# Performance work log

Hardware: AMD Instinct MI355X
Metric: run time of the kernel (lower is better)

## Reference

```python
import jax, jax.numpy as jnp
import numpy as np

N, E = 100000, 800000
D_IN, D_H, D_EMB = 64, 64, 64
L, S = 2, 4
NOISE_SCALE, MIN_U = 0.1, 1e-6


def _xavier(k, shape):
    lim = float(np.sqrt(6.0 / (shape[0] + shape[1])))
    return jax.random.uniform(k, shape, jnp.float32, -lim, lim)


def setup_inputs():
    key = jax.random.key(0)
    ks = jax.random.split(key, 7)
    x = jax.random.normal(ks[0], (N, D_IN), jnp.float32)
    edge_index = jax.random.randint(ks[1], (2, E), 0, N)
    parent_mask = jax.random.bernoulli(ks[2], 0.7, (E,))
    Wi = _xavier(ks[3], (D_IN, D_H))
    bi = jnp.zeros((D_H,), jnp.float32)
    msg_W = jnp.stack([_xavier(jax.random.fold_in(ks[4], l), (2 * D_H, D_H)) for l in range(L)])
    msg_b = jnp.zeros((L, D_H), jnp.float32)
    upd_W = jnp.stack([_xavier(jax.random.fold_in(ks[5], l), (2 * D_H, D_H)) for l in range(L)])
    upd_b = jnp.zeros((L, D_H), jnp.float32)
    Wf = _xavier(ks[6], (D_H, D_EMB))
    bf = jnp.zeros((D_EMB,), jnp.float32)
    return dict(x=x, edge_index=edge_index, parent_mask=parent_mask, Wi=Wi, bi=bi,
                msg_W=msg_W, msg_b=msg_b, upd_W=upd_W, upd_b=upd_b, Wf=Wf, bf=bf)


def _gnn(x, src, dst, mask_f, cnt_inv, Wi, bi, msg_W, msg_b, upd_W, upd_b, Wf, bf):
    # input_proj -> relu, then L rounds of (gather -> message linear -> masked
    # scatter-mean -> update linear -> relu), then final_proj.
    h = jax.nn.relu(x @ Wi + bi)
    for l in range(L):
        Wm, Wu = msg_W[l], upd_W[l]
        # message = Linear(concat(x_i, x_j)); x_i = h[dst] (target), x_j = h[src] (source)
        msg = h[dst] @ Wm[:D_H] + h[src] @ Wm[D_H:] + msg_b[l]  # [E, D_H]
        agg = jax.ops.segment_sum(msg * mask_f[:, None], dst, num_segments=N) * cnt_inv[:, None]
        # update = Linear(concat(x, aggr_out))
        h = jax.nn.relu(h @ Wu[:D_H] + agg @ Wu[D_H:] + upd_b[l])
    return h @ Wf + bf  # [N, D_EMB]


def reference(x, edge_index, parent_mask, Wi, bi, msg_W, msg_b, upd_W, upd_b, Wf, bf):
    src, dst = edge_index[0], edge_index[1]
    mask_f = parent_mask.astype(x.dtype)
    # scatter-mean over causal-parent edges only (0 for nodes without parents, as in PyG)
    cnt = jax.ops.segment_sum(mask_f, dst, num_segments=N)
    cnt_inv = 1.0 / jnp.maximum(cnt, 1.0)
    params = (Wi, bi, msg_W, msg_b, upd_W, upd_b, Wf, bf)
    causal_z = _gnn(x, src, dst, mask_f, cnt_inv, *params)
    # Monte Carlo uncertainty: S perturbed causal embeddings, trace of sample covariance
    noise = jax.random.normal(jax.random.key(42), (S, N, D_IN), x.dtype) * NOISE_SCALE
    zs = jax.lax.map(lambda n: _gnn(x + n, src, dst, mask_f, cnt_inv, *params), noise)  # [S, N, D_EMB]
    mean = zs.mean(axis=0)
    u = jnp.sum((zs - mean[None]) ** 2, axis=(0, 2)) / (S - 1)
    u = jnp.maximum(u, MIN_U)
    return causal_z, u
```

## Files before the change

kernel.cpp:

```cpp
#include <hip/hip_runtime.h>
#include <stdint.h>

#define NN 100000
#define EE 800000
#define GEMM_BX 1563
#define WSTR 72
#define SLAB ((size_t)NN * 64)
#define EDGE_CAP 2304

typedef unsigned short u16;
typedef __attribute__((ext_vector_type(8))) short bf16x8;
typedef __attribute__((ext_vector_type(4))) float f32x4;

__device__ __forceinline__ uint32_t f2bf(float f) {
  uint32_t u = __float_as_uint(f);
  return (u + 0x7fffu + ((u >> 16) & 1u)) >> 16;
}

__device__ __forceinline__ void tf_round(uint32_t& x0, uint32_t& x1, int r) {
  x0 += x1;
  x1 = (x1 << r) | (x1 >> (32 - r));
  x1 ^= x0;
}

__device__ __forceinline__ void threefry_0_42(uint32_t c0, uint32_t c1,
                                              uint32_t& o0, uint32_t& o1) {
  const uint32_t ks0 = 0u, ks1 = 42u, ks2 = 0x1BD11BDAu ^ 42u;
  uint32_t x0 = c0 + ks0, x1 = c1 + ks1;
  tf_round(x0, x1, 13); tf_round(x0, x1, 15); tf_round(x0, x1, 26); tf_round(x0, x1, 6);
  x0 += ks1; x1 += ks2 + 1u;
  tf_round(x0, x1, 17); tf_round(x0, x1, 29); tf_round(x0, x1, 16); tf_round(x0, x1, 24);
  x0 += ks2; x1 += ks0 + 2u;
  tf_round(x0, x1, 13); tf_round(x0, x1, 15); tf_round(x0, x1, 26); tf_round(x0, x1, 6);
  x0 += ks0; x1 += ks1 + 3u;
  tf_round(x0, x1, 17); tf_round(x0, x1, 29); tf_round(x0, x1, 16); tf_round(x0, x1, 24);
  x0 += ks1; x1 += ks2 + 4u;
  tf_round(x0, x1, 13); tf_round(x0, x1, 15); tf_round(x0, x1, 26); tf_round(x0, x1, 6);
  x0 += ks2; x1 += ks0 + 5u;
  o0 = x0; o1 = x1;
}

__device__ __forceinline__ float noise_val(int s, int n, int d) {
  uint32_t f = (uint32_t)s * 6400000u + (uint32_t)n * 64u + (uint32_t)d;
  uint32_t o0, o1;
  threefry_0_42(0u, f, o0, o1);
  uint32_t bits = o0 ^ o1;
  float v = __uint_as_float((bits >> 9) | 0x3f800000u) - 1.0f;
  const float LO = -0.99999994f;
  float u = v * 2.0f + LO;
  u = fmaxf(u, LO);
  float w = -__logf(fmaf(-u, u, 1.0f));
  float ww = w - 2.5f;
  float p = 2.81022636e-08f;
  p = fmaf(p, ww, 3.43273939e-07f);
  p = fmaf(p, ww, -3.5233877e-06f);
  p = fmaf(p, ww, -4.39150654e-06f);
  p = fmaf(p, ww, 0.00021858087f);
  p = fmaf(p, ww, -0.00125372503f);
  p = fmaf(p, ww, -0.00417768164f);
  p = fmaf(p, ww, 0.246640727f);
  p = fmaf(p, ww, 1.50140941f);
  if (__any(w >= 5.0f)) {
    float ws = sqrtf(w) - 3.0f;
    float p2 = -0.000200214257f;
    p2 = fmaf(p2, ws, 0.000100950558f);
    p2 = fmaf(p2, ws, 0.00134934322f);
    p2 = fmaf(p2, ws, -0.00367342844f);
    p2 = fmaf(p2, ws, 0.00573950773f);
    p2 = fmaf(p2, ws, -0.0076224613f);
    p2 = fmaf(p2, ws, 0.00943887047f);
    p2 = fmaf(p2, ws, 1.00167406f);
    p2 = fmaf(p2, ws, 2.83297682f);
    p = (w < 5.0f) ? p : p2;
  }
  return 0.141421356f * (p * u);
}

__device__ __forceinline__ int mask_at(const void* m, int e, int mode) {
  if (mode == 0) return ((const int*)m)[e] != 0;
  if (mode == 1) return ((const unsigned char*)m)[e] != 0;
  return ((const float*)m)[e] != 0.0f;
}

__global__ void k_detect(const unsigned* mw, int* mode_out) {
  __shared__ int nonbin, nonfloat;
  if (threadIdx.x == 0) { nonbin = 0; nonfloat = 0; }
  __syncthreads();
  int lb = 0, lf = 0;
  for (int i = threadIdx.x; i < 4096; i += 256) {
    unsigned v = mw[i];
    if (v > 1u) lb = 1;
    if (v != 0u && v != 0x3F800000u) lf = 1;
  }
  if (lb) atomicOr(&nonbin, 1);
  if (lf) atomicOr(&nonfloat, 1);
  __syncthreads();
  if (threadIdx.x == 0)
    mode_out[0] = (nonbin == 0) ? 0 : ((nonfloat == 0) ? 2 : 1);
}

__global__ void k_count(const void* mask, const int* dst, int* cnt, const int* mode_p) {
  int e = blockIdx.x * 256 + threadIdx.x;
  if (e >= EE) return;
  if (mask_at(mask, e, *mode_p)) atomicAdd(&cnt[dst[e]], 1);
}

__global__ void k_scan_a(const int* cnt, int* blockSums) {
  __shared__ int sd[256];
  int t = threadIdx.x;
  int base = blockIdx.x * 1024 + t * 4;
  int s = 0;
  #pragma unroll
  for (int j = 0; j < 4; ++j) {
    int i = base + j;
    if (i < NN) s += cnt[i];
  }
  sd[t] = s;
  __syncthreads();
  for (int off = 128; off > 0; off >>= 1) {
    if (t < off) sd[t] += sd[t + off];
    __syncthreads();
  }
  if (t == 0) blockSums[blockIdx.x] = sd[0];
}

__global__ void k_scan_b(int* blockSums, int nb, int* total_out) {
  __shared__ int sd[128];
  int t = threadIdx.x;
  int v = (t < nb) ? blockSums[t] : 0;
  sd[t] = v;
  __syncthreads();
  for (int off = 1; off < 128; off <<= 1) {
    int x = (t >= off) ? sd[t - off] : 0;
    __syncthreads();
    sd[t] += x;
    __syncthreads();
  }
  if (t < nb) blockSums[t] = sd[t] - v;
  if (t == 0) total_out[0] = sd[127];
}

__global__ void k_scan_c(const int* cnt, const int* blockOffs, int* row_ptr,
                         int* cursor, float* cinv) {
  __shared__ int sd[256];
  int t = threadIdx.x;
  int base = blockIdx.x * 1024 + t * 4;
  int v[4], s = 0;
  #pragma unroll
  for (int j = 0; j < 4; ++j) {
    int i = base + j;
    v[j] = (i < NN) ? cnt[i] : 0;
    s += v[j];
  }
  sd[t] = s;
  __syncthreads();
  for (int off = 1; off < 256; off <<= 1) {
    int x = (t >= off) ? sd[t - off] : 0;
    __syncthreads();
    sd[t] += x;
    __syncthreads();
  }
  int excl = sd[t] - s + blockOffs[blockIdx.x];
  #pragma unroll
  for (int j = 0; j < 4; ++j) {
    int i = base + j;
    if (i < NN) {
      row_ptr[i] = excl;
      cursor[i] = excl;
      cinv[i] = 1.0f / fmaxf((float)v[j], 1.0f);
    }
    excl += v[j];
  }
}

__global__ void k_fill(const void* mask, const int* src, const int* dst,
                       int* cursor, int* col, const int* mode_p) {
  int e = blockIdx.x * 256 + threadIdx.x;
  if (e >= EE) return;
  if (mask_at(mask, e, *mode_p)) {
    int p = atomicAdd(&cursor[dst[e]], 1);
    col[p] = src[e];
  }
}

__global__ void k_prep(const float* msg_W, const float* msg_b, const float* upd_W,
                       const float* Wi, const float* Wf,
                       u16* Wu1T, u16* A1T, u16* A2T, float* C1,
                       u16* WiT, u16* WfT) {
  int t = threadIdx.x;
  int blk = blockIdx.x;
  if (blk >= 128) {
    const float* W = (blk == 128) ? Wi : Wf;
    u16* WT = (blk == 128) ? WiT : WfT;
    for (int o = t; o < 4096; o += 256) {
      int k = o >> 6, n = o & 63;
      WT[n * 64 + k] = (u16)f2bf(W[k * 64 + n]);
    }
    int l = blk - 128;
    const float* Wu2 = upd_W + l * 8192 + 4096;
    if (t < 64) {
      float acc = 0.f;
      for (int j = 0; j < 64; ++j) acc = fmaf(msg_b[l * 64 + j], Wu2[j * 64 + t], acc);
      C1[l * 64 + t] = acc;
    }
    return;
  }
  int l = blk >> 6, b = blk & 63;
  const float* WmT = msg_W + l * 8192;
  const float* WmB = WmT + 4096;
  const float* Wu1 = upd_W + l * 8192;
  const float* Wu2 = Wu1 + 4096;
  __shared__ float sd1[256], sd2[256];
  int a = t & 63, part = t >> 6;
  float a1 = 0.f, a2 = 0.f;
  #pragma unroll
  for (int jj = 0; jj < 16; ++jj) {
    int j = part * 16 + jj;
    float w2 = Wu2[j * 64 + b];
    a1 = fmaf(WmT[a * 64 + j], w2, a1);
    a2 = fmaf(WmB[a * 64 + j], w2, a2);
  }
  sd1[part * 64 + a] = a1;
  sd2[part * 64 + a] = a2;
  __syncthreads();
  if (t < 64) {
    float s1 = sd1[t] + sd1[64 + t] + sd1[128 + t] + sd1[192 + t];
    float s2 = sd2[t] + sd2[64 + t] + sd2[128 + t] + sd2[192 + t];
    int o = l * 4096 + b * 64 + t;
    A1T[o] = (u16)f2bf(s1);
    A2T[o] = (u16)f2bf(s2);
    Wu1T[o] = (u16)f2bf(Wu1[t * 64 + b]);
  }
}

__device__ __forceinline__ void mm4(const u16* lW, int m16, int q,
                                    bf16x8 a0, bf16x8 a1, f32x4 (&acc)[4]) {
  #pragma unroll
  for (int nt = 0; nt < 4; ++nt) {
    const u16* wp = lW + (nt * 16 + m16) * WSTR + q * 8;
    bf16x8 b0 = *(const bf16x8*)(wp);
    bf16x8 b1 = *(const bf16x8*)(wp + 32);
    acc[nt] = __builtin_amdgcn_mfma_f32_16x16x32_bf16(a0, b0, acc[nt], 0, 0, 0);
    acc[nt] = __builtin_amdgcn_mfma_f32_16x16x32_bf16(a1, b1, acc[nt], 0, 0, 0);
  }
}

__device__ __forceinline__ void stage_W(const u16* __restrict__ WT, u16* lW) {
  int t = threadIdx.x;
  int r = t >> 2, seg = (t & 3) * 16;
  const uint4* p = (const uint4*)(WT + r * 64 + seg);
  uint4 a = p[0], b = p[1];
  *(uint4*)(lW + r * WSTR + seg) = a;
  *(uint4*)(lW + r * WSTR + seg + 8) = b;
}

__device__ __forceinline__ void stage_H(const u16* __restrict__ Hin, int R0, u16* lT) {
  int t = threadIdx.x;
  int r = t >> 2, seg = (t & 3) * 16;
  int gr = R0 + r;
  uint4 a = {0, 0, 0, 0}, b = {0, 0, 0, 0};
  if (gr < NN) {
    const uint4* p = (const uint4*)(Hin + (size_t)gr * 64 + seg);
    a = p[0]; b = p[1];
  }
  *(uint4*)(lT + r * WSTR + seg) = a;
  *(uint4*)(lT + r * WSTR + seg + 8) = b;
}

__global__ __launch_bounds__(256) void k_input(const float* __restrict__ x,
                                               const u16* __restrict__ WiT,
                                               const float* __restrict__ bi,
                                               u16* __restrict__ HoutB) {
  __shared__ __align__(16) u16 lT[64 * WSTR];
  __shared__ __align__(16) u16 lW[64 * WSTR];
  __shared__ float lB[64];
  int t = threadIdx.x;
  int R0 = blockIdx.x * 64;
  int inst = blockIdx.y;
  u16* Hout = HoutB + (size_t)inst * SLAB;
  {
    int r = t >> 2, seg = (t & 3) * 16;
    int gr = R0 + r;
    float v[16];
    if (gr < NN) {
      const float4* xp = (const float4*)(x + (size_t)gr * 64 + seg);
      #pragma unroll
      for (int qq = 0; qq < 4; ++qq) {
        float4 f = xp[qq];
        v[qq * 4 + 0] = f.x; v[qq * 4 + 1] = f.y;
        v[qq * 4 + 2] = f.z; v[qq * 4 + 3] = f.w;
      }
      if (inst > 0) {
        int s = inst - 1;
        #pragma unroll
        for (int j = 0; j < 16; ++j) v[j] += noise_val(s, gr, seg + j);
      }
    } else {
      #pragma unroll
      for (int j = 0; j < 16; ++j) v[j] = 0.f;
    }
    uint32_t pk[8];
    #pragma unroll
    for (int j = 0; j < 8; ++j)
      pk[j] = f2bf(v[2 * j]) | (f2bf(v[2 * j + 1]) << 16);
    uint4 A = {pk[0], pk[1], pk[2], pk[3]};
    uint4 B = {pk[4], pk[5], pk[6], pk[7]};
    *(uint4*)(lT + r * WSTR + seg) = A;
    *(uint4*)(lT + r * WSTR + seg + 8) = B;
  }
  stage_W(WiT, lW);
  if (t < 64) lB[t] = bi[t];
  __syncthreads();
  int l = t & 63, w = t >> 6;
  int m16 = l & 15, q = l >> 4;
  const u16* aRow = lT + (w * 16 + m16) * WSTR + q * 8;
  bf16x8 fa0 = *(const bf16x8*)(aRow);
  bf16x8 fa1 = *(const bf16x8*)(aRow + 32);
  f32x4 acc[4] = {{0.f, 0.f, 0.f, 0.f}, {0.f, 0.f, 0.f, 0.f},
                  {0.f, 0.f, 0.f, 0.f}, {0.f, 0.f, 0.f, 0.f}};
  mm4(lW, m16, q, fa0, fa1, acc);
  #pragma unroll
  for (int nt = 0; nt < 4; ++nt) {
    int c = nt * 16 + m16;
    #pragma unroll
    for (int r_ = 0; r_ < 4; ++r_) {
      int row = w * 16 + q * 4 + r_;
      int gr = R0 + row;
      if (gr < NN) {
        float vv = fmaxf(acc[nt][r_] + lB[c], 0.f);
        Hout[(size_t)gr * 64 + c] = (u16)f2bf(vv);
      }
    }
  }
}

__global__ __launch_bounds__(256) void k_layer(const u16* __restrict__ HinB,
                                               u16* __restrict__ HoutB,
                                               const int* __restrict__ row_ptr,
                                               const int* __restrict__ col,
                                               const float* __restrict__ cinv,
                                               const u16* __restrict__ Wu1T,
                                               const u16* __restrict__ A1T,
                                               const u16* __restrict__ A2T,
                                               const float* __restrict__ b0,
                                               const float* __restrict__ c1) {
  __shared__ __align__(16) u16 lS0[64 * WSTR];
  __shared__ __align__(16) u16 lS1[64 * WSTR];
  __shared__ __align__(16) u16 lW[64 * WSTR];
  __shared__ float lB[128];
  __shared__ float lG[64];
  __shared__ int   lRP[65];
  int* lEdge = (int*)lW;

  int t = threadIdx.x;
  int R0 = blockIdx.x * 64;
  int instBase = blockIdx.y * 2;
  bool two = (instBase + 1) < 5;
  const u16* Hin0 = HinB + (size_t)instBase * SLAB;
  const u16* Hin1 = Hin0 + (two ? SLAB : 0);
  u16* Hout0 = HoutB + (size_t)instBase * SLAB;
  u16* Hout1 = Hout0 + SLAB;

  if (t < 65) {
    int idx = R0 + t;
    if (idx > NN) idx = NN;
    lRP[t] = row_ptr[idx];
  }
  if (t < 64) {
    lB[t] = b0[t];
    lB[64 + t] = c1[t];
  }
  __syncthreads();

  int e0 = lRP[0];
  int nE = lRP[64] - e0;
  bool inLds = (nE <= EDGE_CAP);
  if (inLds) {
    for (int i = t; i < nE; i += 256) lEdge[i] = col[e0 + i];
  }
  if (t < 64) lG[t] = (lRP[t + 1] > lRP[t]) ? 1.f : 0.f;
  __syncthreads();

  {
    int sub = t >> 3, lane8 = t & 7;
    int f0 = lane8 * 8;
    const u16* hb0 = Hin0 + f0;
    const u16* hb1 = Hin1 + f0;
    #pragma unroll
    for (int bb = 0; bb < 2; ++bb) {
      int r = bb * 32 + sub;
      int n = R0 + r;
      float g[8], h[8];
      #pragma unroll
      for (int j = 0; j < 8; ++j) { g[j] = 0.f; h[j] = 0.f; }
      if (n < NN) {
        int e = lRP[r], end = lRP[r + 1];
        int last = end - 1;
        for (; e < end; e += 4) {
          int idx4[4];
          #pragma unroll
          for (int j = 0; j < 4; ++j) {
            int ee = e + j;
            ee = (ee < last) ? ee : last;
            idx4[j] = inLds ? lEdge[ee - e0] : col[ee];
          }
          uint4 P[4];
          #pragma unroll
          for (int j = 0; j < 4; ++j)
            P[j] = *(const uint4*)(hb0 + ((unsigned)idx4[j] << 6));
          uint4 Q[4];
          if (two) {
            #pragma unroll
            for (int j = 0; j < 4; ++j)
              Q[j] = *(const uint4*)(hb1 + ((unsigned)idx4[j] << 6));
          }
          #pragma unroll
          for (int j = 1; j < 4; ++j) {
            bool ok = (e + j) < end;
            P[j].x = ok ? P[j].x : 0u;
            P[j].y = ok ? P[j].y : 0u;
            P[j].z = ok ? P[j].z : 0u;
            P[j].w = ok ? P[j].w : 0u;
            if (two) {
              Q[j].x = ok ? Q[j].x : 0u;
              Q[j].y = ok ? Q[j].y : 0u;
              Q[j].z = ok ? Q[j].z : 0u;
              Q[j].w = ok ? Q[j].w : 0u;
            }
          }
          #pragma unroll
          for (int j = 0; j < 4; ++j) {
            uint4 v = P[j];
            g[0] += __uint_as_float(v.x << 16);
            g[1] += __uint_as_float(v.x & 0xffff0000u);
            g[2] += __uint_as_float(v.y << 16);
            g[3] += __uint_as_float(v.y & 0xffff0000u);
            g[4] += __uint_as_float(v.z << 16);
            g[5] += __uint_as_float(v.z & 0xffff0000u);
            g[6] += __uint_as_float(v.w << 16);
            g[7] += __uint_as_float(v.w & 0xffff0000u);
          }
          if (two) {
            #pragma unroll
            for (int j = 0; j < 4; ++j) {
              uint4 v = Q[j];
              h[0] += __uint_as_float(v.x << 16);
              h[1] += __uint_as_float(v.x & 0xffff0000u);
              h[2] += __uint_as_float(v.y << 16);
              h[3] += __uint_as_float(v.y & 0xffff0000u);
              h[4] += __uint_as_float(v.z << 16);
              h[5] += __uint_as_float(v.z & 0xffff0000u);
              h[6] += __uint_as_float(v.w << 16);
              h[7] += __uint_as_float(v.w & 0xffff0000u);
            }
          }
        }
        float ci = cinv[n];
        #pragma unroll
        for (int j = 0; j < 8; ++j) { g[j] *= ci; h[j] *= ci; }
      }
      uint4 pk;
      pk.x = f2bf(g[0]) | (f2bf(g[1]) << 16);
      pk.y = f2bf(g[2]) | (f2bf(g[3]) << 16);
      pk.z = f2bf(g[4]) | (f2bf(g[5]) << 16);
      pk.w = f2bf(g[6]) | (f2bf(g[7]) << 16);
      *(uint4*)(lS0 + r * WSTR + f0) = pk;
      if (two) {
        uint4 pk2;
        pk2.x = f2bf(h[0]) | (f2bf(h[1]) << 16);
        pk2.y = f2bf(h[2]) | (f2bf(h[3]) << 16);
        pk2.z = f2bf(h[4]) | (f2bf(h[5]) << 16);
        pk2.w = f2bf(h[6]) | (f2bf(h[7]) << 16);
        *(uint4*)(lS1 + r * WSTR + f0) = pk2;
      }
    }
  }
  __syncthreads();

  int l = t & 63, w = t >> 6;
  int m16 = l & 15, q = l >> 4;
  int arow = w * 16 + m16;
  int gra = R0 + arow;
  bf16x8 zz = {0, 0, 0, 0, 0, 0, 0, 0};
  bf16x8 fa0_0 = zz, fa1_0 = zz, fa0_1 = zz, fa1_1 = zz;
  if (gra < NN) {
    const u16* ap = Hin0 + (size_t)gra * 64 + q * 8;
    fa0_0 = *(const bf16x8*)(ap);
    fa1_0 = *(const bf16x8*)(ap + 32);
    if (two) {
      const u16* ap1 = Hin1 + (size_t)gra * 64 + q * 8;
      fa0_1 = *(const bf16x8*)(ap1);
      fa1_1 = *(const bf16x8*)(ap1 + 32);
    }
  }

  stage_W(Wu1T, lW);
  __syncthreads();

  float gA = lG[arow];
  f32x4 acc0[4] = {{0.f, 0.f, 0.f, 0.f}, {0.f, 0.f, 0.f, 0.f},
                   {0.f, 0.f, 0.f, 0.f}, {0.f, 0.f, 0.f, 0.f}};
  f32x4 acc1[4] = {{0.f, 0.f, 0.f, 0.f}, {0.f, 0.f, 0.f, 0.f},
                   {0.f, 0.f, 0.f, 0.f}, {0.f, 0.f, 0.f, 0.f}};
  mm4(lW, m16, q, fa0_0, fa1_0, acc0);
  if (two) mm4(lW, m16, q, fa0_1, fa1_1, acc1);
  __syncthreads();
  stage_W(A1T, lW);
  __syncthreads();
  {
    bf16x8 ga0 = (gA != 0.f) ? fa0_0 : zz;
    bf16x8 ga1 = (gA != 0.f) ? fa1_0 : zz;
    mm4(lW, m16, q, ga0, ga1, acc0);
    if (two) {
      bf16x8 gb0 = (gA != 0.f) ? fa0_1 : zz;
      bf16x8 gb1 = (gA != 0.f) ? fa1_1 : zz;
      mm4(lW, m16, q, gb0, gb1, acc1);
    }
  }
  __syncthreads();
  stage_W(A2T, lW);
  __syncthreads();
  {
    const u16* sRow = lS0 + arow * WSTR + q * 8;
    bf16x8 fs0 = *(const bf16x8*)(sRow);
    bf16x8 fs1 = *(const bf16x8*)(sRow + 32);
    mm4(lW, m16, q, fs0, fs1, acc0);
    if (two) {
      const u16* sRow1 = lS1 + arow * WSTR + q * 8;
      bf16x8 ft0 = *(const bf16x8*)(sRow1);
      bf16x8 ft1 = *(const bf16x8*)(sRow1 + 32);
      mm4(lW, m16, q, ft0, ft1, acc1);
    }
  }
  #pragma unroll
  for (int nt = 0; nt < 4; ++nt) {
    int c = nt * 16 + m16;
    #pragma unroll
    for (int r_ = 0; r_ < 4; ++r_) {
      int row = w * 16 + q * 4 + r_;
      int gr = R0 + row;
      if (gr < NN) {
        float bias = lB[c] + lG[row] * lB[64 + c];
        float v0 = fmaxf(acc0[nt][r_] + bias, 0.f);
        Hout0[(size_t)gr * 64 + c] = (u16)f2bf(v0);
        if (two) {
          float v1 = fmaxf(acc1[nt][r_] + bias, 0.f);
          Hout1[(size_t)gr * 64 + c] = (u16)f2bf(v1);
        }
      }
    }
  }
}

__global__ __launch_bounds__(256) void k_final(const u16* __restrict__ HinB,
                                               const u16* __restrict__ WfT,
                                               const float* __restrict__ bfv,
                                               float* __restrict__ outCausal,
                                               float* __restrict__ out_u) {
  __shared__ __align__(16) u16 lT[64 * WSTR];
  __shared__ __align__(16) u16 lW[64 * WSTR];
  __shared__ float lB[64];
  int t = threadIdx.x;
  int R0 = blockIdx.x * 64;
  stage_W(WfT, lW);
  if (t < 64) lB[t] = bfv[t];
  int l = t & 63, w = t >> 6;
  int m16 = l & 15, q = l >> 4;
  float s1[16], s2[16];
  #pragma unroll
  for (int j = 0; j < 16; ++j) { s1[j] = 0.f; s2[j] = 0.f; }

  for (int inst = 0; inst < 5; ++inst) {
    __syncthreads();
    stage_H(HinB + (size_t)inst * SLAB, R0, lT);
    __syncthreads();
    const u16* aRow = lT + (w * 16 + m16) * WSTR + q * 8;
    bf16x8 fa0 = *(const bf16x8*)(aRow);
    bf16x8 fa1 = *(const bf16x8*)(aRow + 32);
    f32x4 acc[4] = {{0.f, 0.f, 0.f, 0.f}, {0.f, 0.f, 0.f, 0.f},
                    {0.f, 0.f, 0.f, 0.f}, {0.f, 0.f, 0.f, 0.f}};
    mm4(lW, m16, q, fa0, fa1, acc);
    #pragma unroll
    for (int nt = 0; nt < 4; ++nt) {
      int c = nt * 16 + m16;
      #pragma unroll
      for (int r_ = 0; r_ < 4; ++r_) {
        float z = acc[nt][r_] + lB[c];
        if (inst == 0) {
          int gr = R0 + w * 16 + q * 4 + r_;
          if (gr < NN) outCausal[(size_t)gr * 64 + c] = z;
        } else {
          s1[nt * 4 + r_] += z;
          s2[nt * 4 + r_] = fmaf(z, z, s2[nt * 4 + r_]);
        }
      }
    }
  }
  #pragma unroll
  for (int r_ = 0; r_ < 4; ++r_) {
    float pr = 0.f;
    #pragma unroll
    for (int nt = 0; nt < 4; ++nt) {
      float a = s1[nt * 4 + r_];
      pr += s2[nt * 4 + r_] - 0.25f * a * a;
    }
    #pragma unroll
    for (int msk = 1; msk < 16; msk <<= 1)
      pr += __shfl_xor(pr, msk, 64);
    if (m16 == 0) {
      int gr = R0 + w * 16 + q * 4 + r_;
      if (gr < NN) out_u[gr] = fmaxf(pr * (1.0f / 3.0f), 1e-6f);
    }
  }
}

extern "C" void kernel_launch(void* const* d_in, const int* in_sizes, int n_in,
                              void* d_out, int out_size, void* d_ws, size_t ws_size,
                              hipStream_t stream) {
  const float* x      = (const float*)d_in[0];
  const int*   eidx   = (const int*)d_in[1];
  const void*  mask   = d_in[2];
  const float* Wi     = (const float*)d_in[3];
  const float* bi     = (const float*)d_in[4];
  const float* msg_W  = (const float*)d_in[5];
  const float* msg_b  = (const float*)d_in[6];
  const float* upd_W  = (const float*)d_in[7];
  const float* upd_b  = (const float*)d_in[8];
  const float* Wf     = (const float*)d_in[9];
  const float* bfv    = (const float*)d_in[10];

  const int* src = eidx;
  const int* dst = eidx + EE;

  char* ws = (char*)d_ws;
  size_t off = 0;
  auto alloc = [&](size_t bytes) -> void* {
    void* p = ws + off;
    off += (bytes + 255) & ~(size_t)255;
    return p;
  };

  int*   cnt     = (int*)alloc(NN * sizeof(int));
  float* cinv    = (float*)alloc(NN * sizeof(float));
  int*   row_ptr = (int*)alloc((NN + 1) * sizeof(int));
  int*   cursor  = (int*)alloc(NN * sizeof(int));
  int*   col     = (int*)alloc(EE * sizeof(int));
  int*   bsums   = (int*)alloc(128 * sizeof(int));
  int*   mode_p  = (int*)alloc(sizeof(int));
  u16*   Wu1T    = (u16*)alloc(2 * 4096 * sizeof(u16));
  u16*   A1T     = (u16*)alloc(2 * 4096 * sizeof(u16));
  u16*   A2T     = (u16*)alloc(2 * 4096 * sizeof(u16));
  u16*   WiT     = (u16*)alloc(4096 * sizeof(u16));
  u16*   WfT     = (u16*)alloc(4096 * sizeof(u16));
  float* C1      = (float*)alloc(2 * 64 * sizeof(float));
  u16*   HA      = (u16*)alloc(5 * SLAB * sizeof(u16));
  u16*   HB      = (u16*)alloc(5 * SLAB * sizeof(u16));

  float* out_causal = (float*)d_out;
  float* out_u      = (float*)d_out + SLAB;

  k_detect<<<1, 256, 0, stream>>>((const unsigned*)mask, mode_p);
  hipMemsetAsync(cnt, 0, NN * sizeof(int), stream);
  k_count<<<EE / 256, 256, 0, stream>>>(mask, dst, cnt, mode_p);
  const int SCAN_BLKS = (NN + 1023) / 1024;
  k_scan_a<<<SCAN_BLKS, 256, 0, stream>>>(cnt, bsums);
  k_scan_b<<<1, 128, 0, stream>>>(bsums, SCAN_BLKS, row_ptr + NN);
  k_scan_c<<<SCAN_BLKS, 256, 0, stream>>>(cnt, bsums, row_ptr, cursor, cinv);
  k_fill<<<EE / 256, 256, 0, stream>>>(mask, src, dst, cursor, col, mode_p);

  k_prep<<<130, 256, 0, stream>>>(msg_W, msg_b, upd_W, Wi, Wf,
                                  Wu1T, A1T, A2T, C1, WiT, WfT);

  dim3 g5(GEMM_BX, 5);
  dim3 gl(GEMM_BX, 3);
  k_input<<<g5, 256, 0, stream>>>(x, WiT, bi, HA);
  k_layer<<<gl, 256, 0, stream>>>(HA, HB, row_ptr, col, cinv,
                                  Wu1T, A1T, A2T, upd_b, C1);
  k_layer<<<gl, 256, 0, stream>>>(HB, HA, row_ptr, col, cinv,
                                  Wu1T + 4096, A1T + 4096, A2T + 4096,
                                  upd_b + 64, C1 + 64);
  k_final<<<GEMM_BX, 256, 0, stream>>>(HA, WfT, bfv, out_causal, out_u);

  (void)in_sizes; (void)n_in; (void)out_size; (void)ws_size;
}
```

Baseline: 434.4 us.

## Fuse CSR build passes with input projection into interleaved mega-kernels

Merges the edge-count atomics with the first input-projection tiles and the weight-prep work into one launch, and the CSR fill atomics with the remaining input-projection tiles into a second launch. Even and odd blocks are interleaved so memory-bound atomic work and MFMA-based projection tiles can run on the GPU at the same time. Small prep work (mode detect, Wi/Wf transpose, C1) moves into a tiny pre-kernel. The input-projection loading is also rewritten to read x straight into MFMA fragment registers instead of staging through LDS. This cuts launch count and idle tails but adds divergent block roles and more complex index mapping.

```diff
diff --git a/kernel.cpp b/kernel.cpp
--- a/kernel.cpp
+++ b/kernel.cpp
@@ -7,6 +7,9 @@
 #define WSTR 72
 #define SLAB ((size_t)NN * 64)
 #define EDGE_CAP 2304
+
+#define MA_TOTAL 6379
+#define MB_TOTAL 7814
 
 typedef unsigned short u16;
 typedef __attribute__((ext_vector_type(8))) short bf16x8;
@@ -82,27 +85,44 @@
   return ((const float*)m)[e] != 0.0f;
 }
 
-__global__ void k_detect(const unsigned* mw, int* mode_out) {
-  __shared__ int nonbin, nonfloat;
-  if (threadIdx.x == 0) { nonbin = 0; nonfloat = 0; }
-  __syncthreads();
-  int lb = 0, lf = 0;
-  for (int i = threadIdx.x; i < 4096; i += 256) {
-    unsigned v = mw[i];
-    if (v > 1u) lb = 1;
-    if (v != 0u && v != 0x3F800000u) lf = 1;
-  }
-  if (lb) atomicOr(&nonbin, 1);
-  if (lf) atomicOr(&nonfloat, 1);
-  __syncthreads();
-  if (threadIdx.x == 0)
-    mode_out[0] = (nonbin == 0) ? 0 : ((nonfloat == 0) ? 2 : 1);
-}
-
-__global__ void k_count(const void* mask, const int* dst, int* cnt, const int* mode_p) {
-  int e = blockIdx.x * 256 + threadIdx.x;
-  if (e >= EE) return;
-  if (mask_at(mask, e, *mode_p)) atomicAdd(&cnt[dst[e]], 1);
+__global__ void k_pre(const unsigned* mw, int* mode_out,
+                      const float* Wi, const float* Wf,
+                      const float* msg_b, const float* upd_W,
+                      u16* WiT, u16* WfT, float* C1) {
+  int b = blockIdx.x, t = threadIdx.x;
+  if (b == 0) {
+    __shared__ int nonbin, nonfloat;
+    if (t == 0) { nonbin = 0; nonfloat = 0; }
+    __syncthreads();
+    int lb = 0, lf = 0;
+    for (int i = t; i < 4096; i += 256) {
+      unsigned v = mw[i];
+      if (v > 1u) lb = 1;
+      if (v != 0u && v != 0x3F800000u) lf = 1;
+    }
+    if (lb) atomicOr(&nonbin, 1);
+    if (lf) atomicOr(&nonfloat, 1);
+    __syncthreads();
+    if (t == 0)
+      mode_out[0] = (nonbin == 0) ? 0 : ((nonfloat == 0) ? 2 : 1);
+    return;
+  }
+  if (b <= 2) {
+    const float* W = (b == 1) ? Wi : Wf;
+    u16* WT = (b == 1) ? WiT : WfT;
+    for (int o = t; o < 4096; o += 256) {
+      int k = o >> 6, n = o & 63;
+      WT[n * 64 + k] = (u16)f2bf(W[k * 64 + n]);
+    }
+    return;
+  }
+  int l = b - 3;
+  const float* Wu2 = upd_W + l * 8192 + 4096;
+  if (t < 64) {
+    float acc = 0.f;
+    for (int j = 0; j < 64; ++j) acc = fmaf(msg_b[l * 64 + j], Wu2[j * 64 + t], acc);
+    C1[l * 64 + t] = acc;
+  }
 }
 
 __global__ void k_scan_a(const int* cnt, int* blockSums) {
@@ -173,44 +193,135 @@
   }
 }
 
-__global__ void k_fill(const void* mask, const int* src, const int* dst,
-                       int* cursor, int* col, const int* mode_p) {
-  int e = blockIdx.x * 256 + threadIdx.x;
-  if (e >= EE) return;
-  if (mask_at(mask, e, *mode_p)) {
-    int p = atomicAdd(&cursor[dst[e]], 1);
-    col[p] = src[e];
-  }
-}
-
-__global__ void k_prep(const float* msg_W, const float* msg_b, const float* upd_W,
-                       const float* Wi, const float* Wf,
-                       u16* Wu1T, u16* A1T, u16* A2T, float* C1,
-                       u16* WiT, u16* WfT) {
-  int t = threadIdx.x;
-  int blk = blockIdx.x;
-  if (blk >= 128) {
-    const float* W = (blk == 128) ? Wi : Wf;
-    u16* WT = (blk == 128) ? WiT : WfT;
-    for (int o = t; o < 4096; o += 256) {
-      int k = o >> 6, n = o & 63;
-      WT[n * 64 + k] = (u16)f2bf(W[k * 64 + n]);
-    }
-    int l = blk - 128;
-    const float* Wu2 = upd_W + l * 8192 + 4096;
-    if (t < 64) {
-      float acc = 0.f;
-      for (int j = 0; j < 64; ++j) acc = fmaf(msg_b[l * 64 + j], Wu2[j * 64 + t], acc);
-      C1[l * 64 + t] = acc;
-    }
+__device__ __forceinline__ void mm4(const u16* lW, int m16, int q,
+                                    bf16x8 a0, bf16x8 a1, f32x4 (&acc)[4]) {
+  #pragma unroll
+  for (int nt = 0; nt < 4; ++nt) {
+    const u16* wp = lW + (nt * 16 + m16) * WSTR + q * 8;
+    bf16x8 b0 = *(const bf16x8*)(wp);
+    bf16x8 b1 = *(const bf16x8*)(wp + 32);
+    acc[nt] = __builtin_amdgcn_mfma_f32_16x16x32_bf16(a0, b0, acc[nt], 0, 0, 0);
+    acc[nt] = __builtin_amdgcn_mfma_f32_16x16x32_bf16(a1, b1, acc[nt], 0, 0, 0);
+  }
+}
+
+__device__ __forceinline__ void stage_W(const u16* __restrict__ WT, u16* lW) {
+  int t = threadIdx.x;
+  int r = t >> 2, seg = (t & 3) * 16;
+  const uint4* p = (const uint4*)(WT + r * 64 + seg);
+  uint4 a = p[0], b = p[1];
+  *(uint4*)(lW + r * WSTR + seg) = a;
+  *(uint4*)(lW + r * WSTR + seg + 8) = b;
+}
+
+__device__ __forceinline__ void stage_H(const u16* __restrict__ Hin, int R0, u16* lT) {
+  int t = threadIdx.x;
+  int r = t >> 2, seg = (t & 3) * 16;
+  int gr = R0 + r;
+  uint4 a = {0, 0, 0, 0}, b = {0, 0, 0, 0};
+  if (gr < NN) {
+    const uint4* p = (const uint4*)(Hin + (size_t)gr * 64 + seg);
+    a = p[0]; b = p[1];
+  }
+  *(uint4*)(lT + r * WSTR + seg) = a;
+  *(uint4*)(lT + r * WSTR + seg + 8) = b;
+}
+
+__device__ __forceinline__ void input_block(int tile, int inst,
+                                            const float* __restrict__ x,
+                                            const u16* __restrict__ WiT,
+                                            const float* __restrict__ bi,
+                                            u16* __restrict__ HoutB,
+                                            u16* lW, float* lB) {
+  int t = threadIdx.x;
+  stage_W(WiT, lW);
+  if (t < 64) lB[t] = bi[t];
+  int R0 = tile * 64;
+  int l = t & 63, w = t >> 6;
+  int m16 = l & 15, q = l >> 4;
+  int arow = w * 16 + m16;
+  int gra = R0 + arow;
+  float v[16];
+  if (gra < NN) {
+    const float4* p0 = (const float4*)(x + (size_t)gra * 64 + q * 8);
+    const float4* p1 = (const float4*)(x + (size_t)gra * 64 + q * 8 + 32);
+    float4 a = p0[0], b = p0[1], c = p1[0], d = p1[1];
+    v[0] = a.x;  v[1] = a.y;  v[2] = a.z;  v[3] = a.w;
+    v[4] = b.x;  v[5] = b.y;  v[6] = b.z;  v[7] = b.w;
+    v[8] = c.x;  v[9] = c.y;  v[10] = c.z; v[11] = c.w;
+    v[12] = d.x; v[13] = d.y; v[14] = d.z; v[15] = d.w;
+    if (inst > 0) {
+      int s = inst - 1;
+      #pragma unroll
+      for (int j = 0; j < 8; ++j) v[j] += noise_val(s, gra, q * 8 + j);
+      #pragma unroll
+      for (int j = 0; j < 8; ++j) v[8 + j] += noise_val(s, gra, q * 8 + 32 + j);
+    }
+  } else {
+    #pragma unroll
+    for (int j = 0; j < 16; ++j) v[j] = 0.f;
+  }
+  union UB { uint32_t u[4]; bf16x8 vv; };
+  UB ua, ub;
+  #pragma unroll
+  for (int jj = 0; jj < 4; ++jj) {
+    ua.u[jj] = f2bf(v[2 * jj]) | (f2bf(v[2 * jj + 1]) << 16);
+    ub.u[jj] = f2bf(v[8 + 2 * jj]) | (f2bf(v[8 + 2 * jj + 1]) << 16);
+  }
+  __syncthreads();
+  f32x4 acc[4] = {{0.f, 0.f, 0.f, 0.f}, {0.f, 0.f, 0.f, 0.f},
+                  {0.f, 0.f, 0.f, 0.f}, {0.f, 0.f, 0.f, 0.f}};
+  mm4(lW, m16, q, ua.vv, ub.vv, acc);
+  u16* Hout = HoutB + (size_t)inst * SLAB;
+  #pragma unroll
+  for (int nt = 0; nt < 4; ++nt) {
+    int c = nt * 16 + m16;
+    #pragma unroll
+    for (int r_ = 0; r_ < 4; ++r_) {
+      int row = w * 16 + q * 4 + r_;
+      int gr = R0 + row;
+      if (gr < NN) {
+        float z = fmaxf(acc[nt][r_] + lB[c], 0.f);
+        Hout[(size_t)gr * 64 + c] = (u16)f2bf(z);
+      }
+    }
+  }
+}
+
+__global__ __launch_bounds__(256) void k_megaA(
+    const void* __restrict__ mask, const int* __restrict__ dst,
+    int* __restrict__ cnt, const int* __restrict__ mode_p,
+    const float* __restrict__ x, const u16* __restrict__ WiT,
+    const float* __restrict__ bi, u16* __restrict__ HoutB,
+    const float* __restrict__ msg_W, const float* __restrict__ upd_W,
+    u16* __restrict__ Wu1T, u16* __restrict__ A1T, u16* __restrict__ A2T) {
+  __shared__ __align__(16) u16 lW[64 * WSTR];
+  __shared__ float lB[64];
+  int t = threadIdx.x;
+  int bid = blockIdx.x;
+
+  if (bid < 6250) {
+    if ((bid & 1) == 0) {
+      int e = (bid >> 1) * 256 + t;
+      if (e < EE && mask_at(mask, e, *mode_p)) atomicAdd(&cnt[dst[e]], 1);
+      return;
+    }
+    int idx = bid >> 1;
+    input_block(idx % GEMM_BX, idx / GEMM_BX, x, WiT, bi, HoutB, lW, lB);
     return;
   }
+  if (bid == 6250) {
+    input_block(3125 % GEMM_BX, 3125 / GEMM_BX, x, WiT, bi, HoutB, lW, lB);
+    return;
+  }
+  int blk = bid - 6251;
   int l = blk >> 6, b = blk & 63;
   const float* WmT = msg_W + l * 8192;
   const float* WmB = WmT + 4096;
   const float* Wu1 = upd_W + l * 8192;
   const float* Wu2 = Wu1 + 4096;
-  __shared__ float sd1[256], sd2[256];
+  float* sd1 = (float*)lW;
+  float* sd2 = sd1 + 256;
   int a = t & 63, part = t >> 6;
   float a1 = 0.f, a2 = 0.f;
   #pragma unroll
@@ -233,105 +344,32 @@
   }
 }
 
-__device__ __forceinline__ void mm4(const u16* lW, int m16, int q,
-                                    bf16x8 a0, bf16x8 a1, f32x4 (&acc)[4]) {
-  #pragma unroll
-  for (int nt = 0; nt < 4; ++nt) {
-    const u16* wp = lW + (nt * 16 + m16) * WSTR + q * 8;
-    bf16x8 b0 = *(const bf16x8*)(wp);
-    bf16x8 b1 = *(const bf16x8*)(wp + 32);
-    acc[nt] = __builtin_amdgcn_mfma_f32_16x16x32_bf16(a0, b0, acc[nt], 0, 0, 0);
-    acc[nt] = __builtin_amdgcn_mfma_f32_16x16x32_bf16(a1, b1, acc[nt], 0, 0, 0);
-  }
-}
-
-__device__ __forceinline__ void stage_W(const u16* __restrict__ WT, u16* lW) {
-  int t = threadIdx.x;
-  int r = t >> 2, seg = (t & 3) * 16;
-  const uint4* p = (const uint4*)(WT + r * 64 + seg);
-  uint4 a = p[0], b = p[1];
-  *(uint4*)(lW + r * WSTR + seg) = a;
-  *(uint4*)(lW + r * WSTR + seg + 8) = b;
-}
-
-__device__ __forceinline__ void stage_H(const u16* __restrict__ Hin, int R0, u16* lT) {
-  int t = threadIdx.x;
-  int r = t >> 2, seg = (t & 3) * 16;
-  int gr = R0 + r;
-  uint4 a = {0, 0, 0, 0}, b = {0, 0, 0, 0};
-  if (gr < NN) {
-    const uint4* p = (const uint4*)(Hin + (size_t)gr * 64 + seg);
-    a = p[0]; b = p[1];
-  }
-  *(uint4*)(lT + r * WSTR + seg) = a;
-  *(uint4*)(lT + r * WSTR + seg + 8) = b;
-}
-
-__global__ __launch_bounds__(256) void k_input(const float* __restrict__ x,
-                                               const u16* __restrict__ WiT,
-                                               const float* __restrict__ bi,
-                                               u16* __restrict__ HoutB) {
-  __shared__ __align__(16) u16 lT[64 * WSTR];
+__global__ __launch_bounds__(256) void k_megaB(
+    const void* __restrict__ mask, const int* __restrict__ src,
+    const int* __restrict__ dst, int* __restrict__ cursor,
+    int* __restrict__ col, const int* __restrict__ mode_p,
+    const float* __restrict__ x, const u16* __restrict__ WiT,
+    const float* __restrict__ bi, u16* __restrict__ HoutB) {
   __shared__ __align__(16) u16 lW[64 * WSTR];
   __shared__ float lB[64];
   int t = threadIdx.x;
-  int R0 = blockIdx.x * 64;
-  int inst = blockIdx.y;
-  u16* Hout = HoutB + (size_t)inst * SLAB;
-  {
-    int r = t >> 2, seg = (t & 3) * 16;
-    int gr = R0 + r;
-    float v[16];
-    if (gr < NN) {
-      const float4* xp = (const float4*)(x + (size_t)gr * 64 + seg);
-      #pragma unroll
-      for (int qq = 0; qq < 4; ++qq) {
-        float4 f = xp[qq];
-        v[qq * 4 + 0] = f.x; v[qq * 4 + 1] = f.y;
-        v[qq * 4 + 2] = f.z; v[qq * 4 + 3] = f.w;
+  int bid = blockIdx.x;
+
+  int idx;
+  if (bid < 6250) {
+    if ((bid & 1) == 0) {
+      int e = (bid >> 1) * 256 + t;
+      if (e < EE && mask_at(mask, e, *mode_p)) {
+        int p = atomicAdd(&cursor[dst[e]], 1);
+        col[p] = src[e];
       }
-      if (inst > 0) {
-        int s = inst - 1;
-        #pragma unroll
-        for (int j = 0; j < 16; ++j) v[j] += noise_val(s, gr, seg + j);
-      }
-    } else {
-      #pragma unroll
-      for (int j = 0; j < 16; ++j) v[j] = 0.f;
-    }
-    uint32_t pk[8];
-    #pragma unroll
-    for (int j = 0; j < 8; ++j)
-      pk[j] = f2bf(v[2 * j]) | (f2bf(v[2 * j + 1]) << 16);
-    uint4 A = {pk[0], pk[1], pk[2], pk[3]};
-    uint4 B = {pk[4], pk[5], pk[6], pk[7]};
-    *(uint4*)(lT + r * WSTR + seg) = A;
-    *(uint4*)(lT + r * WSTR + seg + 8) = B;
-  }
-  stage_W(WiT, lW);
-  if (t < 64) lB[t] = bi[t];
-  __syncthreads();
-  int l = t & 63, w = t >> 6;
-  int m16 = l & 15, q = l >> 4;
-  const u16* aRow = lT + (w * 16 + m16) * WSTR + q * 8;
-  bf16x8 fa0 = *(const bf16x8*)(aRow);
-  bf16x8 fa1 = *(const bf16x8*)(aRow + 32);
-  f32x4 acc[4] = {{0.f, 0.f, 0.f, 0.f}, {0.f, 0.f, 0.f, 0.f},
-                  {0.f, 0.f, 0.f, 0.f}, {0.f, 0.f, 0.f, 0.f}};
-  mm4(lW, m16, q, fa0, fa1, acc);
-  #pragma unroll
-  for (int nt = 0; nt < 4; ++nt) {
-    int c = nt * 16 + m16;
-    #pragma unroll
-    for (int r_ = 0; r_ < 4; ++r_) {
-      int row = w * 16 + q * 4 + r_;
-      int gr = R0 + row;
-      if (gr < NN) {
-        float vv = fmaxf(acc[nt][r_] + lB[c], 0.f);
-        Hout[(size_t)gr * 64 + c] = (u16)f2bf(vv);
-      }
-    }
-  }
+      return;
+    }
+    idx = bid >> 1;
+  } else {
+    idx = 3125 + (bid - 6250);
+  }
+  input_block(idx % GEMM_BX, 2 + idx / GEMM_BX, x, WiT, bi, HoutB, lW, lB);
 }
 
 __global__ __launch_bounds__(256) void k_layer(const u16* __restrict__ HinB,
@@ -659,21 +697,23 @@
   float* out_causal = (float*)d_out;
   float* out_u      = (float*)d_out + SLAB;
 
-  k_detect<<<1, 256, 0, stream>>>((const unsigned*)mask, mode_p);
+  k_pre<<<5, 256, 0, stream>>>((const unsigned*)mask, mode_p, Wi, Wf,
+                               msg_b, upd_W, WiT, WfT, C1);
   hipMemsetAsync(cnt, 0, NN * sizeof(int), stream);
-  k_count<<<EE / 256, 256, 0, stream>>>(mask, dst, cnt, mode_p);
+
+  k_megaA<<<MA_TOTAL, 256, 0, stream>>>(mask, dst, cnt, mode_p,
+                                        x, WiT, bi, HA,
+                                        msg_W, upd_W, Wu1T, A1T, A2T);
+
   const int SCAN_BLKS = (NN + 1023) / 1024;
   k_scan_a<<<SCAN_BLKS, 256, 0, stream>>>(cnt, bsums);
   k_scan_b<<<1, 128, 0, stream>>>(bsums, SCAN_BLKS, row_ptr + NN);
   k_scan_c<<<SCAN_BLKS, 256, 0, stream>>>(cnt, bsums, row_ptr, cursor, cinv);
-  k_fill<<<EE / 256, 256, 0, stream>>>(mask, src, dst, cursor, col, mode_p);
-
-  k_prep<<<130, 256, 0, stream>>>(msg_W, msg_b, upd_W, Wi, Wf,
-                                  Wu1T, A1T, A2T, C1, WiT, WfT);
-
-  dim3 g5(GEMM_BX, 5);
+
+  k_megaB<<<MB_TOTAL, 256, 0, stream>>>(mask, src, dst, cursor, col, mode_p,
+                                        x, WiT, bi, HA);
+
   dim3 gl(GEMM_BX, 3);
-  k_input<<<g5, 256, 0, stream>>>(x, WiT, bi, HA);
   k_layer<<<gl, 256, 0, stream>>>(HA, HB, row_ptr, col, cinv,
                                   Wu1T, A1T, A2T, upd_b, C1);
   k_layer<<<gl, 256, 0, stream>>>(HB, HA, row_ptr, col, cinv,
```

Result: no change. 435.3 us (+0.2%).
